# Kernel tuning notes

Hardware: AMD Instinct MI355X
Metric: run time of the kernel (lower is better)

## Reference

```python
import jax, jax.numpy as jnp
import numpy as np

LEAKY = 0.2
BN_EPS = 1e-5
N_NODES = 50000
IN_F = 128
HID = 64
HEADS = 2
N_EDGES = 1600000


def _bn(x, gamma, beta):
    # BatchNorm1d in training mode: batch statistics over the node dim
    mu = jnp.mean(x, axis=0)
    var = jnp.mean((x - mu) ** 2, axis=0)
    return (x - mu) * jax.lax.rsqrt(var + BN_EPS) * gamma + beta


def _gat(x, src, dst, W, a_src, a_dst, bias, n):
    # W: [F_in, H*F], a_src/a_dst: [H, F]
    H, F = a_src.shape
    h = (x @ W).reshape(n, H, F)                      # [N,H,F]
    es = jnp.einsum('nhf,hf->nh', h, a_src)           # [N,H]
    ed = jnp.einsum('nhf,hf->nh', h, a_dst)           # [N,H]
    e = jax.nn.leaky_relu(es[src] + ed[dst], LEAKY)   # [E,H]
    m = jax.ops.segment_max(e, dst, num_segments=n)   # stable softmax per dst
    p = jnp.exp(e - m[dst])
    s = jax.ops.segment_sum(p, dst, num_segments=n)
    alpha = p / s[dst]                                # [E,H]
    out = jax.ops.segment_sum(h[src] * alpha[:, :, None], dst, num_segments=n)
    return out.reshape(n, H * F) + bias


def setup_inputs() -> dict:
    key = jax.random.key(0)
    ks = jax.random.split(key, 32)
    HF = HID * HEADS  # 128

    def g(k, shape, scale=0.1):
        return jax.random.normal(k, shape, dtype=jnp.float32) * scale

    inp = {
        'x': jax.random.normal(ks[0], (N_NODES, IN_F), dtype=jnp.float32),
        'edge_index': jax.random.randint(ks[1], (2, N_EDGES), 0, N_NODES, dtype=jnp.int64),
        # layer 1
        'W1': g(ks[2], (IN_F, HF)), 'as1': g(ks[3], (HEADS, HID)), 'ad1': g(ks[4], (HEADS, HID)),
        'gb1': jnp.zeros((HF,), jnp.float32),
        'lw1': g(ks[5], (IN_F, HF)), 'lb1': jnp.zeros((HF,), jnp.float32),
        'bg1': jnp.ones((IN_F,), jnp.float32), 'bb1': jnp.zeros((IN_F,), jnp.float32),
        # layer 2
        'W2': g(ks[6], (HF, HF)), 'as2': g(ks[7], (HEADS, HID)), 'ad2': g(ks[8], (HEADS, HID)),
        'gb2': jnp.zeros((HF,), jnp.float32),
        'lw2': g(ks[9], (HF, HF)), 'lb2': jnp.zeros((HF,), jnp.float32),
        'bg2': jnp.ones((HF,), jnp.float32), 'bb2': jnp.zeros((HF,), jnp.float32),
        # layer 3 (heads=1, out=2)
        'W3': g(ks[10], (HF, 2)), 'as3': g(ks[11], (1, 2)), 'ad3': g(ks[12], (1, 2)),
        'gb3': jnp.zeros((2,), jnp.float32),
        'lw3': g(ks[13], (HF, 2)), 'lb3': jnp.zeros((2,), jnp.float32),
        'bg3': jnp.ones((HF,), jnp.float32), 'bb3': jnp.zeros((HF,), jnp.float32),
    }
    return inp


def reference(x, edge_index,
              W1, as1, ad1, gb1, lw1, lb1, bg1, bb1,
              W2, as2, ad2, gb2, lw2, lb2, bg2, bb2,
              W3, as3, ad3, gb3, lw3, lb3, bg3, bb3):
    n = x.shape[0]
    loop = jnp.arange(n, dtype=edge_index.dtype)  # self-loops (PyG GAT default)
    src = jnp.concatenate([edge_index[0], loop])
    dst = jnp.concatenate([edge_index[1], loop])

    h = _bn(x, bg1, bb1)
    h = jax.nn.relu(h @ lw1 + lb1 + _gat(h, src, dst, W1, as1, ad1, gb1, n))
    h = _bn(h, bg2, bb2)
    h = jax.nn.relu(h @ lw2 + lb2 + _gat(h, src, dst, W2, as2, ad2, gb2, n))
    h = _bn(h, bg3, bb3)
    h = jax.nn.relu(h @ lw3 + lb3 + _gat(h, src, dst, W3, as3, ad3, gb3, n))
    return h
```

## Files before the change

kernel.cpp:

```cpp
#include <hip/hip_runtime.h>

#define LEAKY 0.2f
#define BN_EPS 1e-5f
#define BCHUNK 8192

typedef __bf16 v8bf __attribute__((ext_vector_type(8)));
typedef float v16f __attribute__((ext_vector_type(16)));
typedef float v2f __attribute__((ext_vector_type(2)));

__device__ __forceinline__ float wsum(float v) {
#pragma unroll
  for (int o = 32; o > 0; o >>= 1) v += __shfl_xor(v, o, 64);
  return v;
}

__device__ __forceinline__ float blo(unsigned u) { return __uint_as_float(u << 16); }
__device__ __forceinline__ float bhi(unsigned u) { return __uint_as_float(u & 0xffff0000u); }
__device__ __forceinline__ v2f bpair(unsigned u) {
  v2f r; r.x = __uint_as_float(u << 16); r.y = __uint_as_float(u & 0xffff0000u); return r;
}
__device__ __forceinline__ unsigned pack_bf16(float a, float b) {
  unsigned ua = __float_as_uint(a), ub = __float_as_uint(b);
  ua = (ua + 0x7fffu + ((ua >> 16) & 1u)) >> 16;
  ub = (ub + 0x7fffu + ((ub >> 16) & 1u)) >> 16;
  return ua | (ub << 16);
}
__device__ __forceinline__ unsigned short bf16of(float a) {
  unsigned ua = __float_as_uint(a);
  return (unsigned short)((ua + 0x7fffu + ((ua >> 16) & 1u)) >> 16);
}

__device__ __forceinline__ int edge_at(const void* ei, int is64, long long i) {
  return is64 ? (int)((const long long*)ei)[i] : ((const int*)ei)[i];
}


__device__ __forceinline__ void binA_body(int blk, const void* ei, int N, int E, int M,
                                          int nb, int nblk, int* counts, int* lds) {
  int* hist = lds;
  int* sflag = lds + 1024;
  int tid = threadIdx.x;
  if (tid < 64) {
    const long long* p = (const long long*)ei;
    long long v = p[tid];
    int bad = (v < 0 || v >= (long long)N) ? 1 : 0;
    unsigned long long mres = __ballot(bad);
    if (tid == 0) *sflag = (mres == 0ull) ? 1 : 0;
  }
  for (int j = tid; j < nb; j += 256) hist[j] = 0;
  __syncthreads();
  int is64 = *sflag;
  long long base = (long long)blk * BCHUNK;
  int cnt = (int)min((long long)BCHUNK, (long long)M - base);
  for (int i = tid; i < cnt; i += 256) {
    long long g = base + i;
    int d = (g < E) ? edge_at(ei, is64, (long long)E + g) : (int)(g - E);
    atomicAdd(&hist[d >> 7], 1);
  }
  __syncthreads();
  for (int j = tid; j < nb; j += 256) counts[(size_t)j * nblk + blk] = hist[j];
}

__device__ __forceinline__ void binC_body(int blk, const void* ei, int N, int E, int M,
                                          int nb, int nblk, const int* counts,
                                          unsigned* tmp, int* lds) {
  int* cur = lds;
  int* sflag = lds + 1024;
  int tid = threadIdx.x;
  if (tid < 64) {
    const long long* p = (const long long*)ei;
    long long v = p[tid];
    int bad = (v < 0 || v >= (long long)N) ? 1 : 0;
    unsigned long long mres = __ballot(bad);
    if (tid == 0) *sflag = (mres == 0ull) ? 1 : 0;
  }
  for (int j = tid; j < nb; j += 256) cur[j] = counts[(size_t)j * nblk + blk];
  __syncthreads();
  int is64 = *sflag;
  long long base = (long long)blk * BCHUNK;
  int cnt = (int)min((long long)BCHUNK, (long long)M - base);
  for (int i = tid; i < cnt; i += 256) {
    long long g = base + i;
    int s, d;
    if (g < E) { s = edge_at(ei, is64, g); d = edge_at(ei, is64, (long long)E + g); }
    else       { s = d = (int)(g - E); }
    int pos = atomicAdd(&cur[d >> 7], 1);
    tmp[pos] = ((unsigned)s << 7) | (unsigned)(d & 127);
  }
}

#define MM_SMEM (32 * 136 * 2 + 128 * 4 + 128 * 4)

__device__ __forceinline__ void mm_body(int blk, const void* xin, int packed,
    const float* stats, const float* gamma, const float* beta,
    const unsigned short* Bp, unsigned* hb, unsigned* linp,
    float* es, float* ed, int N, char* smem) {
  unsigned short* Al = (unsigned short*)smem;
  float* scl_s = (float*)(smem + 8704);
  float* sht_s = (float*)(smem + 8704 + 512);
  int tid = threadIdx.x;
  int lane = tid & 63;
  int w = tid >> 6;
  int rowBase = blk * 32;

  if (tid < 128) {
    float s = 0.f, s2 = 0.f;
#pragma unroll
    for (int r = 0; r < 8; ++r) {
      s += stats[r * 256 + tid];
      s2 += stats[r * 256 + 128 + tid];
    }
    float inv_n = 1.0f / (float)N;
    float mu = s * inv_n;
    float var = s2 * inv_n - mu * mu;
    float rs = rsqrtf(var + BN_EPS);
    float sc = gamma[tid] * rs;
    scl_s[tid] = sc;
    sht_s[tid] = beta[tid] - mu * sc;
  }

  v8bf bfrag[2][8];
#pragma unroll
  for (int t = 0; t < 2; ++t)
#pragma unroll
    for (int s = 0; s < 8; ++s) {
      int fi = ((2 * w + t) * 8 + s) * 64 + lane;
      bfrag[t][s] = *(const v8bf*)&Bp[(size_t)fi * 8];
    }
  __syncthreads();

  if (!packed) {
    const float* x = (const float*)xin;
    for (int q = tid; q < 32 * 32; q += 256) {
      int r = q >> 5, k4 = (q & 31) * 4;
      int row = rowBase + r;
      float4 v = make_float4(0.f, 0.f, 0.f, 0.f);
      if (row < N) v = *(const float4*)&x[(size_t)row * 128 + k4];
      unsigned p0 = pack_bf16(v.x * scl_s[k4] + sht_s[k4], v.y * scl_s[k4 + 1] + sht_s[k4 + 1]);
      unsigned p1 = pack_bf16(v.z * scl_s[k4 + 2] + sht_s[k4 + 2], v.w * scl_s[k4 + 3] + sht_s[k4 + 3]);
      *(uint2*)&Al[r * 136 + k4] = make_uint2(p0, p1);
    }
  } else {
    const unsigned* xp = (const unsigned*)xin;
    for (int q = tid; q < 32 * 16; q += 256) {
      int r = q >> 4, g = q & 15;
      int row = rowBase + r;
      uint4 u = make_uint4(0u, 0u, 0u, 0u);
      if (row < N) u = *(const uint4*)&xp[(size_t)row * 64 + g * 4];
      int f = g * 8;
      uint4 o;
      o.x = pack_bf16(blo(u.x) * scl_s[f] + sht_s[f], bhi(u.x) * scl_s[f + 1] + sht_s[f + 1]);
      o.y = pack_bf16(blo(u.y) * scl_s[f + 2] + sht_s[f + 2], bhi(u.y) * scl_s[f + 3] + sht_s[f + 3]);
      o.z = pack_bf16(blo(u.z) * scl_s[f + 4] + sht_s[f + 4], bhi(u.z) * scl_s[f + 5] + sht_s[f + 5]);
      o.w = pack_bf16(blo(u.w) * scl_s[f + 6] + sht_s[f + 6], bhi(u.w) * scl_s[f + 7] + sht_s[f + 7]);
      *(uint4*)&Al[r * 136 + f] = o;
    }
  }
  __syncthreads();

  int m = lane & 31, half = lane >> 5;
  v8bf afrag[8];
#pragma unroll
  for (int s = 0; s < 8; ++s)
    afrag[s] = *(const v8bf*)&Al[m * 136 + s * 16 + half * 8];

  v16f acc0 = {}, acc1 = {};
#pragma unroll
  for (int s = 0; s < 8; ++s) {
    acc0 = __builtin_amdgcn_mfma_f32_32x32x16_bf16(afrag[s], bfrag[0][s], acc0, 0, 0, 0);
    acc1 = __builtin_amdgcn_mfma_f32_32x32x16_bf16(afrag[s], bfrag[1][s], acc1, 0, 0, 0);
  }

  v16f acc2 = {};
  if (w == 0) {
#pragma unroll
    for (int s = 0; s < 8; ++s) {
      v8bf besf = *(const v8bf*)&Bp[(size_t)((64 + s) * 64 + lane) * 8];
      acc2 = __builtin_amdgcn_mfma_f32_32x32x16_bf16(afrag[s], besf, acc2, 0, 0, 0);
    }
  }

  int mlo = half * 4;
  int t0 = 2 * w, t1 = 2 * w + 1;
#pragma unroll
  for (int r = 0; r < 16; ++r) {
    int row = (r & 3) + 8 * (r >> 2) + mlo;
    int node = rowBase + row;
    float a0 = acc0[r], a1 = acc1[r];
    float b0 = __shfl_xor(a0, 1, 64);
    float b1 = __shfl_xor(a1, 1, 64);
    if (node < N && !(lane & 1)) {
      if (t0 < 4) {
        hb[(size_t)node * 64 + (t0 * 16 + (m >> 1))] = pack_bf16(a0, b0);
        hb[(size_t)node * 64 + (t1 * 16 + (m >> 1))] = pack_bf16(a1, b1);
      } else {
        linp[(size_t)node * 64 + ((t0 - 4) * 16 + (m >> 1))] = pack_bf16(a0, b0);
        linp[(size_t)node * 64 + ((t1 - 4) * 16 + (m >> 1))] = pack_bf16(a1, b1);
      }
    }
    if (w == 0 && m < 4 && node < N) {
      float v = acc2[r];
      if (m < 2) es[2 * node + (m & 1)] = v;
      else       ed[2 * node + (m & 1)] = v;
    }
  }
}


__global__ __launch_bounds__(256) void k_prepA(
    const float* __restrict__ W1, const float* __restrict__ LW1,
    const float* __restrict__ W2, const float* __restrict__ LW2,
    const float* __restrict__ as1, const float* __restrict__ ad1,
    const float* __restrict__ as2, const float* __restrict__ ad2,
    const float* __restrict__ x, int N,
    unsigned short* __restrict__ Bp1, unsigned short* __restrict__ Bp2,
    float* __restrict__ stats1,
    const void* ei, int E, int M, int nb, int nblk, int* counts) {
  __shared__ __align__(16) int lds[1025];
  int blk = blockIdx.x;
  int tid = threadIdx.x;
  if (blk >= 1058) { binA_body(blk - 1058, ei, N, E, M, nb, nblk, counts, lds); return; }
  if (blk >= 34) {
    int b = blk - 34;
    int f = tid & 127;
    int half = tid >> 7;
    float s = 0.f, s2 = 0.f;
    for (int r = b + half * 1024; r < N; r += 2048) {
      float v = x[(size_t)r * 128 + f];
      s += v; s2 += v * v;
    }
    float* rep = stats1 + (size_t)(b & 7) * 256;
    atomicAdd(&rep[f], s);
    atomicAdd(&rep[128 + f], s2);
    return;
  }
  if (blk >= 32) {
    float (*wes)[4] = (float(*)[4])lds;
    const float* W = (blk == 32) ? W1 : W2;
    const float* as_ = (blk == 32) ? as1 : as2;
    const float* ad_ = (blk == 32) ? ad1 : ad2;
    unsigned short* Bp = (blk == 32) ? Bp1 : Bp2;
#pragma unroll
    for (int it = 0; it < 2; ++it) {
      int k = tid & 127;
      int c = (tid >> 7) + 2 * it;
      const float* a = (c < 2) ? as_ : ad_;
      int hb2 = (c & 1) * 64;
      float sum = 0.f;
      for (int f = 0; f < 64; ++f) sum += W[k * 128 + hb2 + f] * a[hb2 + f];
      wes[k][c] = sum;
    }
    __syncthreads();
    for (int fr = tid; fr < 512; fr += 256) {
      int lane = fr & 63, s = fr >> 6;
      int n = lane & 31;
      int k0 = s * 16 + (lane >> 5) * 8;
      unsigned short tb[8];
#pragma unroll
      for (int j = 0; j < 8; ++j)
        tb[j] = bf16of((n < 4) ? wes[k0 + j][n] : 0.f);
      uint4 pk;
      pk.x = (unsigned)tb[0] | ((unsigned)tb[1] << 16);
      pk.y = (unsigned)tb[2] | ((unsigned)tb[3] << 16);
      pk.z = (unsigned)tb[4] | ((unsigned)tb[5] << 16);
      pk.w = (unsigned)tb[6] | ((unsigned)tb[7] << 16);
      int fi = (64 + s) * 64 + lane;
      *(uint4*)&Bp[(size_t)fi * 8] = pk;
    }
    return;
  }
  const float* W  = (blk < 16) ? W1 : W2;
  const float* LW = (blk < 16) ? LW1 : LW2;
  unsigned short* Bp = (blk < 16) ? Bp1 : Bp2;
  int fi = (blk & 15) * 256 + tid;
  int lane = fi & 63, s = (fi >> 6) & 7, t = fi >> 9;
  int n = t * 32 + (lane & 31);
  int k0 = s * 16 + (lane >> 5) * 8;
  unsigned short tb[8];
#pragma unroll
  for (int j = 0; j < 8; ++j) {
    int k = k0 + j;
    float v = (n < 128) ? W[k * 128 + n] : LW[k * 128 + (n - 128)];
    tb[j] = bf16of(v);
  }
  uint4 pk;
  pk.x = (unsigned)tb[0] | ((unsigned)tb[1] << 16);
  pk.y = (unsigned)tb[2] | ((unsigned)tb[3] << 16);
  pk.z = (unsigned)tb[4] | ((unsigned)tb[5] << 16);
  pk.w = (unsigned)tb[6] | ((unsigned)tb[7] << 16);
  *(uint4*)&Bp[(size_t)fi * 8] = pk;
}

__global__ __launch_bounds__(1024) void k_binScan(int* counts, int total_entries) {
  __shared__ int part[1024];
  int tid = threadIdx.x;
  int per = (total_entries + 1023) / 1024;
  int lo = tid * per;
  int hi = lo + per; if (hi > total_entries) hi = total_entries;
  int s = 0;
  int i = lo;
  for (; i + 8 <= hi; i += 8) {
    int c0 = counts[i], c1 = counts[i + 1], c2 = counts[i + 2], c3 = counts[i + 3];
    int c4 = counts[i + 4], c5 = counts[i + 5], c6 = counts[i + 6], c7 = counts[i + 7];
    s += ((c0 + c1) + (c2 + c3)) + ((c4 + c5) + (c6 + c7));
  }
  for (; i < hi; ++i) s += counts[i];
  part[tid] = s;
  __syncthreads();
  for (int off = 1; off < 1024; off <<= 1) {
    int add = (tid >= off) ? part[tid - off] : 0;
    __syncthreads();
    part[tid] += add;
    __syncthreads();
  }
  int run = (tid == 0) ? 0 : part[tid - 1];
  i = lo;
  for (; i + 8 <= hi; i += 8) {
    int c0 = counts[i], c1 = counts[i + 1], c2 = counts[i + 2], c3 = counts[i + 3];
    int c4 = counts[i + 4], c5 = counts[i + 5], c6 = counts[i + 6], c7 = counts[i + 7];
    counts[i] = run; run += c0;
    counts[i + 1] = run; run += c1;
    counts[i + 2] = run; run += c2;
    counts[i + 3] = run; run += c3;
    counts[i + 4] = run; run += c4;
    counts[i + 5] = run; run += c5;
    counts[i + 6] = run; run += c6;
    counts[i + 7] = run; run += c7;
  }
  for (; i < hi; ++i) {
    int c = counts[i];
    counts[i] = run;
    run += c;
  }
}

__global__ __launch_bounds__(256) void k_mmC(
    const void* __restrict__ xin, int packed,
    const float* __restrict__ stats, const float* __restrict__ gamma, const float* __restrict__ beta,
    const unsigned short* __restrict__ Bp,
    unsigned* __restrict__ hb, unsigned* __restrict__ linp,
    float* __restrict__ es, float* __restrict__ ed, int N, int gmm,
    const void* ei, int E, int M, int nb, int nblk, const int* counts, unsigned* tmp) {
  __shared__ __align__(16) char smem[MM_SMEM];
  int blk = blockIdx.x;
  if (blk < gmm) {
    mm_body(blk, xin, packed, stats, gamma, beta, Bp, hb, linp, es, ed, N, smem);
  } else {
    binC_body(blk - gmm, ei, N, E, M, nb, nblk, counts, tmp, (int*)smem);
  }
}

__global__ __launch_bounds__(256) void k_mm(
    const void* __restrict__ xin, int packed,
    const float* __restrict__ stats, const float* __restrict__ gamma, const float* __restrict__ beta,
    const unsigned short* __restrict__ Bp,
    unsigned* __restrict__ hb, unsigned* __restrict__ linp,
    float* __restrict__ es, float* __restrict__ ed, int N) {
  __shared__ __align__(16) char smem[MM_SMEM];
  mm_body(blockIdx.x, xin, packed, stats, gamma, beta, Bp, hb, linp, es, ed, N, smem);
}

__global__ __launch_bounds__(256) void k_binD(const unsigned* __restrict__ tmp,
                                              const int* __restrict__ counts,
                                              int nb, int nblk, int M, int N,
                                              int* __restrict__ rowptr, int* __restrict__ col) {
  __shared__ int scn[128];
  __shared__ int cur[128];
  int tid = threadIdx.x;
  int j = blockIdx.x;
  int base = counts[(size_t)j * nblk];
  int endv = (j + 1 < nb) ? counts[(size_t)(j + 1) * nblk] : M;
  int bc = endv - base;
  if (tid < 128) scn[tid] = 0;
  __syncthreads();
  for (int i = tid; i < bc; i += 256) atomicAdd(&scn[tmp[base + i] & 127], 1);
  __syncthreads();
  int v = (tid < 128) ? scn[tid] : 0;
  __syncthreads();
  for (int off = 1; off < 128; off <<= 1) {
    int add = (tid >= off && tid < 128) ? scn[tid - off] : 0;
    __syncthreads();
    if (tid < 128) scn[tid] += add;
    __syncthreads();
  }
  if (tid < 128) {
    int excl = scn[tid] - v;
    int d = (j << 7) + tid;
    if (d < N) rowptr[d] = base + excl;
    cur[tid] = base + excl;
  }
  __syncthreads();
  for (int i = tid; i < bc; i += 256) {
    unsigned w = tmp[base + i];
    int pos = atomicAdd(&cur[w & 127], 1);
    col[pos] = (int)(w >> 7);
  }
  if (j == nb - 1 && tid == 0) rowptr[N] = M;
}

__global__ __launch_bounds__(128) void k_bnstats(const unsigned* __restrict__ xp,
                                                 int N, float* sums) {
  int f = threadIdx.x;
  int q = f >> 1, hi = f & 1;
  float s = 0.f, s2 = 0.f;
  for (int r = blockIdx.x; r < N; r += gridDim.x) {
    unsigned u = xp[(size_t)r * 64 + q];
    float v = hi ? bhi(u) : blo(u);
    s += v; s2 += v * v;
  }
  float* rep = sums + (size_t)(blockIdx.x & 7) * 256;
  atomicAdd(&rep[f], s);
  atomicAdd(&rep[128 + f], s2);
}

__global__ __launch_bounds__(256) void k_agg(
    const int* __restrict__ rowptr, const int* __restrict__ col,
    const float* __restrict__ es, const float* __restrict__ ed,
    const unsigned* __restrict__ hb, const unsigned* __restrict__ linp,
    const float* __restrict__ lb, const float* __restrict__ gb,
    unsigned* __restrict__ xoutp, int N) {
  int lane = threadIdx.x & 63;
  int w = threadIdx.x >> 6;
  int d = blockIdx.x * 4 + w;
  if (d >= N) return;
  int start = rowptr[d], end = rowptr[d + 1];
  v2f edv = *(const v2f*)&ed[2 * d];
  int q = lane >> 4;
  int m = lane & 15;
  int head_hi = m >= 8;
  v2f zero = {0.f, 0.f};
  v2f lk = {LEAKY, LEAKY};

  v2f acc[4] = {zero, zero, zero, zero};
  v2f sp = zero;
  int i = start;
  for (; i + 16 <= end; i += 16) {
#pragma unroll
    for (int b = 0; b < 4; ++b) {
      int idx = i + 4 * b + q;
      int s = col[idx];
      v2f ev = *(const v2f*)&es[2 * s];
      uint4 u = *(const uint4*)&hb[(size_t)s * 64 + m * 4];
      v2f e = ev + edv;
      v2f le = __builtin_elementwise_max(e, zero) + lk * __builtin_elementwise_min(e, zero);
      v2f p; p.x = __expf(le.x); p.y = __expf(le.y);
      sp += p;
      float f = head_hi ? p.y : p.x;
      v2f fv = {f, f};
      acc[0] = __builtin_elementwise_fma(fv, bpair(u.x), acc[0]);
      acc[1] = __builtin_elementwise_fma(fv, bpair(u.y), acc[1]);
      acc[2] = __builtin_elementwise_fma(fv, bpair(u.z), acc[2]);
      acc[3] = __builtin_elementwise_fma(fv, bpair(u.w), acc[3]);
    }
  }
  for (; i < end; i += 4) {
    int idx = i + q;
    int valid = idx < end;
    int s = col[valid ? idx : end - 1];
    v2f ev = *(const v2f*)&es[2 * s];
    uint4 u = *(const uint4*)&hb[(size_t)s * 64 + m * 4];
    v2f e = ev + edv;
    v2f le = __builtin_elementwise_max(e, zero) + lk * __builtin_elementwise_min(e, zero);
    v2f p; p.x = __expf(le.x); p.y = __expf(le.y);
    if (!valid) p = zero;
    sp += p;
    float f = head_hi ? p.y : p.x;
    v2f fv = {f, f};
    acc[0] = __builtin_elementwise_fma(fv, bpair(u.x), acc[0]);
    acc[1] = __builtin_elementwise_fma(fv, bpair(u.y), acc[1]);
    acc[2] = __builtin_elementwise_fma(fv, bpair(u.z), acc[2]);
    acc[3] = __builtin_elementwise_fma(fv, bpair(u.w), acc[3]);
  }
#pragma unroll
  for (int k = 0; k < 4; ++k) {
    acc[k].x += __shfl_xor(acc[k].x, 16, 64);
    acc[k].x += __shfl_xor(acc[k].x, 32, 64);
    acc[k].y += __shfl_xor(acc[k].y, 16, 64);
    acc[k].y += __shfl_xor(acc[k].y, 32, 64);
  }
  sp.x += __shfl_xor(sp.x, 16, 64); sp.x += __shfl_xor(sp.x, 32, 64);
  sp.y += __shfl_xor(sp.y, 16, 64); sp.y += __shfl_xor(sp.y, 32, 64);

  if (q == 0) {
    float inv = 1.0f / (head_hi ? sp.y : sp.x);
    uint4 lv = *(const uint4*)&linp[(size_t)d * 64 + m * 4];
    int f8 = 8 * m;
    float4 lb0 = *(const float4*)&lb[f8], lb1 = *(const float4*)&lb[f8 + 4];
    float4 gb0 = *(const float4*)&gb[f8], gb1 = *(const float4*)&gb[f8 + 4];
    float v0 = blo(lv.x) + lb0.x + acc[0].x * inv + gb0.x;
    float v1 = bhi(lv.x) + lb0.y + acc[0].y * inv + gb0.y;
    float v2 = blo(lv.y) + lb0.z + acc[1].x * inv + gb0.z;
    float v3 = bhi(lv.y) + lb0.w + acc[1].y * inv + gb0.w;
    float v4 = blo(lv.z) + lb1.x + acc[2].x * inv + gb1.x;
    float v5 = bhi(lv.z) + lb1.y + acc[2].y * inv + gb1.y;
    float v6 = blo(lv.w) + lb1.z + acc[3].x * inv + gb1.z;
    float v7 = bhi(lv.w) + lb1.w + acc[3].y * inv + gb1.w;
    v0 = v0 > 0.f ? v0 : 0.f; v1 = v1 > 0.f ? v1 : 0.f;
    v2 = v2 > 0.f ? v2 : 0.f; v3 = v3 > 0.f ? v3 : 0.f;
    v4 = v4 > 0.f ? v4 : 0.f; v5 = v5 > 0.f ? v5 : 0.f;
    v6 = v6 > 0.f ? v6 : 0.f; v7 = v7 > 0.f ? v7 : 0.f;
    uint4 o;
    o.x = pack_bf16(v0, v1); o.y = pack_bf16(v2, v3);
    o.z = pack_bf16(v4, v5); o.w = pack_bf16(v6, v7);
    *(uint4*)&xoutp[(size_t)d * 64 + m * 4] = o;
  }
}

__global__ __launch_bounds__(256) void k_l3node(
    const unsigned* __restrict__ xp,
    const float* __restrict__ stats, const float* __restrict__ gamma, const float* __restrict__ beta,
    const float* __restrict__ W3, const float* __restrict__ LW3,
    const float* __restrict__ as3, const float* __restrict__ ad3,
    float* h3, float* lin3, float* es3, float* ed3, int N) {
  int lane = threadIdx.x & 63;
  int n = blockIdx.x * 4 + (threadIdx.x >> 6);
  if (n >= N) return;
  float inv_n = 1.0f / (float)N;
  int f0 = lane, f1 = 64 + lane;
  float su0 = 0.f, sq0 = 0.f, su1 = 0.f, sq1 = 0.f;
#pragma unroll
  for (int r = 0; r < 8; ++r) {
    su0 += stats[r * 256 + f0];  sq0 += stats[r * 256 + 128 + f0];
    su1 += stats[r * 256 + f1];  sq1 += stats[r * 256 + 128 + f1];
  }
  float mu0 = su0 * inv_n;
  float var0 = sq0 * inv_n - mu0 * mu0;
  float rs0 = rsqrtf(var0 + BN_EPS);
  float sc0 = gamma[f0] * rs0, sh0 = beta[f0] - mu0 * sc0;
  float mu1 = su1 * inv_n;
  float var1 = sq1 * inv_n - mu1 * mu1;
  float rs1 = rsqrtf(var1 + BN_EPS);
  float sc1 = gamma[f1] * rs1, sh1 = beta[f1] - mu1 * sc1;

  unsigned ua = xp[(size_t)n * 64 + (lane >> 1)];
  unsigned ub = xp[(size_t)n * 64 + 32 + (lane >> 1)];
  float xv0 = (lane & 1) ? bhi(ua) : blo(ua);
  float xv1 = (lane & 1) ? bhi(ub) : blo(ub);
  float xn0 = xv0 * sc0 + sh0;
  float xn1 = xv1 * sc1 + sh1;

  float2 w0 = *(const float2*)&W3[lane * 2];
  float2 w1 = *(const float2*)&W3[(64 + lane) * 2];
  float2 l0 = *(const float2*)&LW3[lane * 2];
  float2 l1 = *(const float2*)&LW3[(64 + lane) * 2];
  float hc0 = wsum(xn0 * w0.x + xn1 * w1.x);
  float hc1 = wsum(xn0 * w0.y + xn1 * w1.y);
  float lc0 = wsum(xn0 * l0.x + xn1 * l1.x);
  float lc1 = wsum(xn0 * l0.y + xn1 * l1.y);
  if (lane == 0) {
    h3[2 * n] = hc0; h3[2 * n + 1] = hc1;
    lin3[2 * n] = lc0; lin3[2 * n + 1] = lc1;
    es3[n] = hc0 * as3[0] + hc1 * as3[1];
    ed3[n] = hc0 * ad3[0] + hc1 * ad3[1];
  }
}

__global__ __launch_bounds__(256) void k_agg3(
    const int* __restrict__ rowptr, const int* __restrict__ col,
    const float* __restrict__ es, const float* __restrict__ ed,
    const float* __restrict__ h3, const float* __restrict__ lin3,
    const float* __restrict__ lb3, const float* __restrict__ gb3,
    float* __restrict__ out, int N) {
  int lane = threadIdx.x & 63;
  int d = blockIdx.x * 4 + (threadIdx.x >> 6);
  if (d >= N) return;
  int start = rowptr[d], end = rowptr[d + 1];
  float edd = ed[d];
  float ps = 0.f, a0 = 0.f, a1 = 0.f;
  for (int i = start + lane; i < end; i += 64) {
    int s = col[i];
    float e = es[s] + edd; e = e > 0.f ? e : LEAKY * e;
    float p = __expf(e);
    float2 hv = *(const float2*)&h3[2 * s];
    ps += p; a0 += p * hv.x; a1 += p * hv.y;
  }
  ps = wsum(ps); a0 = wsum(a0); a1 = wsum(a1);
  if (lane < 2) {
    float a = (lane == 0 ? a0 : a1) / ps;
    float v = lin3[2 * d + lane] + lb3[lane] + a + gb3[lane];
    out[2 * d + lane] = v > 0.f ? v : 0.f;
  }
}

extern "C" void kernel_launch(void* const* d_in, const int* in_sizes, int n_in,
                              void* d_out, int out_size, void* d_ws, size_t ws_size,
                              hipStream_t stream) {
  const float* x   = (const float*)d_in[0];
  const void*  ei  = d_in[1];
  const float* W1  = (const float*)d_in[2];
  const float* as1 = (const float*)d_in[3];
  const float* ad1 = (const float*)d_in[4];
  const float* gb1 = (const float*)d_in[5];
  const float* lw1 = (const float*)d_in[6];
  const float* lb1 = (const float*)d_in[7];
  const float* bg1 = (const float*)d_in[8];
  const float* bb1 = (const float*)d_in[9];
  const float* W2  = (const float*)d_in[10];
  const float* as2 = (const float*)d_in[11];
  const float* ad2 = (const float*)d_in[12];
  const float* gb2 = (const float*)d_in[13];
  const float* lw2 = (const float*)d_in[14];
  const float* lb2 = (const float*)d_in[15];
  const float* bg2 = (const float*)d_in[16];
  const float* bb2 = (const float*)d_in[17];
  const float* W3  = (const float*)d_in[18];
  const float* as3 = (const float*)d_in[19];
  const float* ad3 = (const float*)d_in[20];
  const float* gb3 = (const float*)d_in[21];
  const float* lw3 = (const float*)d_in[22];
  const float* lb3 = (const float*)d_in[23];
  const float* bg3 = (const float*)d_in[24];
  const float* bb3 = (const float*)d_in[25];
  float* out = (float*)d_out;

  int N = in_sizes[0] / 128;
  int E = in_sizes[1] / 2;
  int M = E + N;
  int nb = (N + 127) >> 7;
  int nblk = (M + BCHUNK - 1) / BCHUNK;

  char* wsp = (char*)d_ws;
  size_t off = 0;
  auto alloc = [&](size_t bytes) -> void* {
    void* p = wsp + off;
    off = (off + bytes + 255) & ~(size_t)255;
    return p;
  };
  int* rowptr   = (int*)alloc(((size_t)N + 1) * 4);
  int* col      = (int*)alloc((size_t)M * 4);
  unsigned* tmp = (unsigned*)alloc((size_t)M * 4);
  int* counts   = (int*)alloc(((size_t)nb * nblk + 1) * 4);
  float* st1    = (float*)alloc(8 * 256 * 4);
  float* st2    = (float*)alloc(8 * 256 * 4);
  float* st3    = (float*)alloc(8 * 256 * 4);
  unsigned short* Bp1 = (unsigned short*)alloc(4608 * 16);
  unsigned short* Bp2 = (unsigned short*)alloc(4608 * 16);
  unsigned* hbp  = (unsigned*)alloc((size_t)N * 64 * 4);
  unsigned* linp = (unsigned*)alloc((size_t)N * 64 * 4);
  unsigned* x2p  = (unsigned*)alloc((size_t)N * 64 * 4);
  float* es    = (float*)alloc((size_t)N * 2 * 4);
  float* edb   = (float*)alloc((size_t)N * 2 * 4);
  float* h3    = (float*)alloc((size_t)N * 2 * 4);
  float* lin3  = (float*)alloc((size_t)N * 2 * 4);
  float* es3   = (float*)alloc((size_t)N * 4);
  float* ed3   = (float*)alloc((size_t)N * 4);
  (void)ws_size; (void)n_in; (void)out_size;

  hipMemsetAsync(st1, 0, 3 * 8 * 256 * 4, stream);

  int gnode = (N + 3) / 4;
  int gmm = (N + 31) / 32;

  k_prepA<<<1058 + nblk, 256, 0, stream>>>(W1, lw1, W2, lw2, as1, ad1, as2, ad2,
                                           x, N, Bp1, Bp2, st1,
                                           ei, E, M, nb, nblk, counts);
  k_binScan<<<1, 1024, 0, stream>>>(counts, nb * nblk);
  k_mmC<<<gmm + nblk, 256, 0, stream>>>(x, 0, st1, bg1, bb1, Bp1, hbp, linp, es, edb, N,
                                        gmm, ei, E, M, nb, nblk, counts, tmp);
  k_binD<<<nb, 256, 0, stream>>>(tmp, counts, nb, nblk, M, N, rowptr, col);

  k_agg<<<gnode, 256, 0, stream>>>(rowptr, col, es, edb, hbp, linp, lb1, gb1, x2p, N);

  k_bnstats<<<1024, 128, 0, stream>>>(x2p, N, st2);
  k_mm<<<gmm, 256, 0, stream>>>(x2p, 1, st2, bg2, bb2, Bp2, hbp, linp, es, edb, N);
  k_agg<<<gnode, 256, 0, stream>>>(rowptr, col, es, edb, hbp, linp, lb2, gb2, x2p, N);

  k_bnstats<<<1024, 128, 0, stream>>>(x2p, N, st3);
  k_l3node<<<gnode, 256, 0, stream>>>(x2p, st3, bg3, bb3, W3, lw3, as3, ad3,
                                      h3, lin3, es3, ed3, N);
  k_agg3<<<gnode, 256, 0, stream>>>(rowptr, col, es3, ed3, h3, lin3, lb3, gb3, out, N);
}
```

Before: 429.3 us.

## Compute edge softmax weights once per lane and aggregate with bf16 dot2

The GAT aggregation kernel now handles edges in chunks of 64. Each lane computes the attention weight for one edge and stages it as bf16 in LDS, together with the source-row offset. A gather loop then processes two edges per quarter-wave and uses v_dot2_f32_bf16 with byte permutes to accumulate pairs. This removes the exp and leaky-relu work that was repeated across 16 lanes and halves the FMA count, at the cost of LDS traffic and bf16 rounding of the weights, which the fp32 normaliser does not see. A binning chunk size is also raised.

```diff
diff --git a/kernel.cpp b/kernel.cpp
--- a/kernel.cpp
+++ b/kernel.cpp
@@ -2,7 +2,7 @@
 
 #define LEAKY 0.2f
 #define BN_EPS 1e-5f
-#define BCHUNK 8192
+#define BCHUNK 32768
 
 typedef __bf16 v8bf __attribute__((ext_vector_type(8)));
 typedef float v16f __attribute__((ext_vector_type(16)));
@@ -28,6 +28,17 @@
 __device__ __forceinline__ unsigned short bf16of(float a) {
   unsigned ua = __float_as_uint(a);
   return (unsigned short)((ua + 0x7fffu + ((ua >> 16) & 1u)) >> 16);
+}
+
+__device__ __forceinline__ float dot2bf(unsigned a, unsigned b, float c) {
+  asm("v_dot2_f32_bf16 %0, %1, %2, %0" : "+v"(c) : "v"(a), "v"(b));
+  return c;
+}
+__device__ __forceinline__ unsigned permlo(unsigned u1, unsigned u2) {
+  return __builtin_amdgcn_perm(u2, u1, 0x05040100u);
+}
+__device__ __forceinline__ unsigned permhi(unsigned u1, unsigned u2) {
+  return __builtin_amdgcn_perm(u2, u1, 0x07060302u);
 }
 
 __device__ __forceinline__ int edge_at(const void* ei, int is64, long long i) {
@@ -419,6 +430,8 @@
     const unsigned* __restrict__ hb, const unsigned* __restrict__ linp,
     const float* __restrict__ lb, const float* __restrict__ gb,
     unsigned* __restrict__ xoutp, int N) {
+  __shared__ unsigned short phb[4][2][64];
+  __shared__ unsigned obuf[4][64];
   int lane = threadIdx.x & 63;
   int w = threadIdx.x >> 6;
   int d = blockIdx.x * 4 + w;
@@ -432,44 +445,41 @@
   v2f lk = {LEAKY, LEAKY};
 
   v2f acc[4] = {zero, zero, zero, zero};
-  v2f sp = zero;
-  int i = start;
-  for (; i + 16 <= end; i += 16) {
-#pragma unroll
-    for (int b = 0; b < 4; ++b) {
-      int idx = i + 4 * b + q;
-      int s = col[idx];
+  v2f spv = zero;
+  unsigned short* ph = &phb[w][0][0];
+  unsigned* oo = obuf[w];
+  int hoff = head_hi ? 64 : 0;
+
+  for (int base = start; base < end; base += 64) {
+    int cnt = end - base; if (cnt > 64) cnt = 64;
+    {
+      int valid = lane < cnt;
+      int s = col[valid ? base + lane : base];
       v2f ev = *(const v2f*)&es[2 * s];
-      uint4 u = *(const uint4*)&hb[(size_t)s * 64 + m * 4];
       v2f e = ev + edv;
       v2f le = __builtin_elementwise_max(e, zero) + lk * __builtin_elementwise_min(e, zero);
       v2f p; p.x = __expf(le.x); p.y = __expf(le.y);
-      sp += p;
-      float f = head_hi ? p.y : p.x;
-      v2f fv = {f, f};
-      acc[0] = __builtin_elementwise_fma(fv, bpair(u.x), acc[0]);
-      acc[1] = __builtin_elementwise_fma(fv, bpair(u.y), acc[1]);
-      acc[2] = __builtin_elementwise_fma(fv, bpair(u.z), acc[2]);
-      acc[3] = __builtin_elementwise_fma(fv, bpair(u.w), acc[3]);
-    }
-  }
-  for (; i < end; i += 4) {
-    int idx = i + q;
-    int valid = idx < end;
-    int s = col[valid ? idx : end - 1];
-    v2f ev = *(const v2f*)&es[2 * s];
-    uint4 u = *(const uint4*)&hb[(size_t)s * 64 + m * 4];
-    v2f e = ev + edv;
-    v2f le = __builtin_elementwise_max(e, zero) + lk * __builtin_elementwise_min(e, zero);
-    v2f p; p.x = __expf(le.x); p.y = __expf(le.y);
-    if (!valid) p = zero;
-    sp += p;
-    float f = head_hi ? p.y : p.x;
-    v2f fv = {f, f};
-    acc[0] = __builtin_elementwise_fma(fv, bpair(u.x), acc[0]);
-    acc[1] = __builtin_elementwise_fma(fv, bpair(u.y), acc[1]);
-    acc[2] = __builtin_elementwise_fma(fv, bpair(u.z), acc[2]);
-    acc[3] = __builtin_elementwise_fma(fv, bpair(u.w), acc[3]);
+      if (!valid) p = zero;
+      spv += p;
+      ph[lane] = bf16of(p.x);
+      ph[64 + lane] = bf16of(p.y);
+      oo[lane] = (unsigned)s * 64u;
+    }
+    for (int i = 0; i < cnt; i += 8) {
+      int e1 = i + 2 * q;
+      unsigned fp = *(const unsigned*)&ph[hoff + e1];
+      uint2 ofs = *(const uint2*)&oo[e1];
+      uint4 u1 = *(const uint4*)&hb[(size_t)ofs.x + m * 4];
+      uint4 u2 = *(const uint4*)&hb[(size_t)ofs.y + m * 4];
+      acc[0].x = dot2bf(fp, permlo(u1.x, u2.x), acc[0].x);
+      acc[0].y = dot2bf(fp, permhi(u1.x, u2.x), acc[0].y);
+      acc[1].x = dot2bf(fp, permlo(u1.y, u2.y), acc[1].x);
+      acc[1].y = dot2bf(fp, permhi(u1.y, u2.y), acc[1].y);
+      acc[2].x = dot2bf(fp, permlo(u1.z, u2.z), acc[2].x);
+      acc[2].y = dot2bf(fp, permhi(u1.z, u2.z), acc[2].y);
+      acc[3].x = dot2bf(fp, permlo(u1.w, u2.w), acc[3].x);
+      acc[3].y = dot2bf(fp, permhi(u1.w, u2.w), acc[3].y);
+    }
   }
 #pragma unroll
   for (int k = 0; k < 4; ++k) {
@@ -478,11 +488,14 @@
     acc[k].y += __shfl_xor(acc[k].y, 16, 64);
     acc[k].y += __shfl_xor(acc[k].y, 32, 64);
   }
-  sp.x += __shfl_xor(sp.x, 16, 64); sp.x += __shfl_xor(sp.x, 32, 64);
-  sp.y += __shfl_xor(sp.y, 16, 64); sp.y += __shfl_xor(sp.y, 32, 64);
+#pragma unroll
+  for (int o = 1; o < 64; o <<= 1) {
+    spv.x += __shfl_xor(spv.x, o, 64);
+    spv.y += __shfl_xor(spv.y, o, 64);
+  }
 
   if (q == 0) {
-    float inv = 1.0f / (head_hi ? sp.y : sp.x);
+    float inv = 1.0f / (head_hi ? spv.y : spv.x);
     uint4 lv = *(const uint4*)&linp[(size_t)d * 64 + m * 4];
     int f8 = 8 * m;
     float4 lb0 = *(const float4*)&lb[f8], lb1 = *(const float4*)&lb[f8 + 4];
```

Result: slower. 472.2 us (+10.0%).
